# Kernel optimization log

Measured on AMD Instinct MI355X. Metric: run time of the kernel, lower is better.

The kernel has to match this reference:

```python
import jax, jax.numpy as jnp
import numpy as np

CLUSTER_TEMP = 5.0


def setup_inputs() -> dict:
    key = jax.random.key(0)
    ks = jax.random.split(key, 8)
    n, d_in, h, d, K = 50000, 512, 1024, 256, 64
    s = lambda f: 1.0 / np.sqrt(f)
    return {
        "x": jax.random.normal(ks[0], (n, d_in), dtype=jnp.float32),
        "W1": jax.random.normal(ks[1], (d_in, h), dtype=jnp.float32) * s(d_in),
        "b1": jnp.zeros((h,), jnp.float32),
        "W2": jax.random.normal(ks[2], (h, h), dtype=jnp.float32) * s(h),
        "b2": jnp.zeros((h,), jnp.float32),
        "W3": jax.random.normal(ks[3], (h, d), dtype=jnp.float32) * s(h),
        "b3": jnp.zeros((d,), jnp.float32),
        "mu_init": jax.random.normal(ks[4], (K, d), dtype=jnp.float32),
        "num_iter": 10,
    }


def reference(x, W1, b1, W2, b2, W3, b3, mu_init, num_iter):
    # MLP embed: ReLU on all but last layer
    h1 = jax.nn.relu(x @ W1 + b1)
    h2 = jax.nn.relu(h1 @ W2 + b2)
    embeds = h2 @ W3 + b3                      # [n, d]

    # row-wise L2 normalize (torch.diag(1/norm) @ data == row scaling)
    data = embeds / jnp.linalg.norm(embeds, axis=1, keepdims=True)

    def step(mu, _):
        dist = data @ mu.T                     # [n, K]
        r = jax.nn.softmax(CLUSTER_TEMP * dist, axis=1)
        cluster_r = r.sum(axis=0)              # [K]
        cluster_mean = jnp.einsum('nk,nd->kd', r, data)  # [K, d]
        new_mu = cluster_mean / cluster_r[:, None]       # diag(1/cluster_r) @ mean
        return new_mu, None

    mu, _ = jax.lax.scan(step, mu_init, None, length=num_iter)
    dist = data @ mu.T
    r = jax.nn.softmax(CLUSTER_TEMP * dist, axis=1)      # forward returns r only
    return r
```

## Files before the change

### kernel.cpp

```cpp
#include <hip/hip_runtime.h>
#include <math.h>

#define CLUSTER_TEMP 5.0f

typedef __attribute__((ext_vector_type(8))) short bf16x8;
typedef __attribute__((ext_vector_type(4))) float f32x4;

__device__ __forceinline__ unsigned short f2bf(float f) {
  unsigned u = __float_as_uint(f);
  u += 0x7fff + ((u >> 16) & 1);
  return (unsigned short)(u >> 16);
}
__device__ __forceinline__ float bf2f(unsigned short s) {
  return __uint_as_float((unsigned)s << 16);
}

typedef const __attribute__((address_space(1))) void* gas_t;
typedef __attribute__((address_space(3))) void* las_t;
__device__ __forceinline__ void gload16(const void* g, void* l) {
  __builtin_amdgcn_global_load_lds((gas_t)g, (las_t)l, 16, 0, 0);
}

__global__ __launch_bounds__(256)
void wprep(const float* __restrict__ W, unsigned short* __restrict__ hi,
           unsigned short* __restrict__ lo, int K, int N)
{
  __shared__ float tile[32][33];
  const int bx = blockIdx.x * 32;
  const int by = blockIdx.y * 32;
  const int tx = threadIdx.x, ty = threadIdx.y;
#pragma unroll
  for (int i = 0; i < 4; ++i)
    tile[ty + i*8][tx] = W[(size_t)(by + ty + i*8)*N + bx + tx];
  __syncthreads();
#pragma unroll
  for (int i = 0; i < 4; ++i) {
    const int nn = bx + ty + i*8;
    const int kk = by + tx;
    const float v = tile[tx][ty + i*8];
    const unsigned short h = f2bf(v);
    hi[(size_t)nn*K + kk] = h;
    lo[(size_t)nn*K + kk] = f2bf(v - bf2f(h));
  }
}

__global__ __launch_bounds__(256)
void xsplit(const float* __restrict__ x, unsigned short* __restrict__ xh,
            unsigned short* __restrict__ xl, long total4)
{
  long i = (long)blockIdx.x*256 + threadIdx.x;
  const long stride = (long)gridDim.x*256;
  for (; i < total4; i += stride) {
    float4 v = ((const float4*)x)[i];
    ushort4 h, lo;
    h.x = f2bf(v.x); lo.x = f2bf(v.x - bf2f(h.x));
    h.y = f2bf(v.y); lo.y = f2bf(v.y - bf2f(h.y));
    h.z = f2bf(v.z); lo.z = f2bf(v.z - bf2f(h.z));
    h.w = f2bf(v.w); lo.w = f2bf(v.w - bf2f(h.w));
    ((ushort4*)xh)[i] = h;
    ((ushort4*)xl)[i] = lo;
  }
}

template<bool RELU, bool PAIR_OUT>
__global__ __launch_bounds__(256, 2)
void gemm_pair(const unsigned short* __restrict__ Ah, const unsigned short* __restrict__ Al,
               const unsigned short* __restrict__ Bh, const unsigned short* __restrict__ Bl,
               const float* __restrict__ bias,
               unsigned short* __restrict__ Ch, unsigned short* __restrict__ Cl,
               float* __restrict__ Cf,
               int M, int N, int K)
{
  __shared__ unsigned short As_h[128][32];
  __shared__ unsigned short As_l[128][32];
  __shared__ unsigned short Bs_h[128][32];
  __shared__ unsigned short Bs_l[128][32];
  const int t = threadIdx.x, l = t & 63, w = t >> 6;
  const int wm = w >> 1, wn = w & 1;
  const int fr = l & 15, fq = l >> 4;

  const int gx = gridDim.x;
  const int total = gx * gridDim.y;
  const int flat = blockIdx.y * gx + blockIdx.x;
  const int q = total >> 3, rmd = total & 7;
  const int xcd = flat & 7, pos = flat >> 3;
  const int nid = (xcd < rmd ? xcd * (q + 1) : rmd * (q + 1) + (xcd - rmd) * q) + pos;
  const int row0 = (nid / gx) * 128;
  const int col0 = (nid % gx) * 128;

  const int srow = l >> 2;
  const int scol = (l & 3) * 8;

  f32x4 acc[4][4];
#pragma unroll
  for (int i = 0; i < 4; ++i)
#pragma unroll
    for (int j = 0; j < 4; ++j) {
      acc[i][j][0]=0.f; acc[i][j][1]=0.f; acc[i][j][2]=0.f; acc[i][j][3]=0.f;
    }

  for (int k0 = 0; k0 < K; k0 += 32) {
    __syncthreads();
#pragma unroll
    for (int j = 0; j < 2; ++j) {
      const int chunk = w*2 + j;
      const int rl = chunk*16 + srow;
      const int ra = min(row0 + rl, M-1);
      const size_t ao = (size_t)ra*K + k0 + scol;
      const size_t bo = (size_t)(col0 + rl)*K + k0 + scol;
      gload16(Ah + ao, &As_h[chunk*16][0]);
      gload16(Al + ao, &As_l[chunk*16][0]);
      gload16(Bh + bo, &Bs_h[chunk*16][0]);
      gload16(Bl + bo, &Bs_l[chunk*16][0]);
    }
    __syncthreads();

    bf16x8 ah[4], al[4], bh[4], bl[4];
#pragma unroll
    for (int i = 0; i < 4; ++i) {
      ah[i] = *(const bf16x8*)&As_h[wm*64 + i*16 + fr][fq*8];
      al[i] = *(const bf16x8*)&As_l[wm*64 + i*16 + fr][fq*8];
      bh[i] = *(const bf16x8*)&Bs_h[wn*64 + i*16 + fr][fq*8];
      bl[i] = *(const bf16x8*)&Bs_l[wn*64 + i*16 + fr][fq*8];
    }
#pragma unroll
    for (int i = 0; i < 4; ++i)
#pragma unroll
      for (int j = 0; j < 4; ++j) {
        acc[i][j] = __builtin_amdgcn_mfma_f32_16x16x32_bf16(ah[i], bh[j], acc[i][j], 0, 0, 0);
        acc[i][j] = __builtin_amdgcn_mfma_f32_16x16x32_bf16(ah[i], bl[j], acc[i][j], 0, 0, 0);
        acc[i][j] = __builtin_amdgcn_mfma_f32_16x16x32_bf16(al[i], bh[j], acc[i][j], 0, 0, 0);
      }
  }

  float bj[4];
#pragma unroll
  for (int j = 0; j < 4; ++j) bj[j] = bias[col0 + wn*64 + j*16 + fr];

#pragma unroll
  for (int i = 0; i < 4; ++i)
#pragma unroll
    for (int qq = 0; qq < 4; ++qq) {
      const int r = row0 + wm*64 + i*16 + fq*4 + qq;
      if (r < M) {
#pragma unroll
        for (int j = 0; j < 4; ++j) {
          float v = acc[i][j][qq] + bj[j];
          if constexpr (RELU) v = fmaxf(v, 0.f);
          const int cidx = col0 + wn*64 + j*16 + fr;
          if constexpr (PAIR_OUT) {
            const unsigned short h = f2bf(v);
            Ch[(size_t)r*N + cidx] = h;
            Cl[(size_t)r*N + cidx] = f2bf(v - bf2f(h));
          } else {
            Cf[(size_t)r*N + cidx] = v;
          }
        }
      }
    }
}

__global__ __launch_bounds__(256)
void normsplit(const float* __restrict__ E,
               unsigned short* __restrict__ dsph, unsigned short* __restrict__ dspl,
               unsigned short* __restrict__ dshT, unsigned short* __restrict__ dslT,
               int n, int nt)
{
  __shared__ float tile[64][260];
  __shared__ float nrm[4][64];
  __shared__ float invr[64];
  const int t = threadIdx.x;
  const int n0 = blockIdx.x * 64;
#pragma unroll
  for (int i = 0; i < 16; ++i) {
    const int flat = t + i*256;
    const int r = flat >> 6, c4 = (flat & 63) * 4;
    const int rg = min(n0 + r, n - 1);
    *(float4*)&tile[r][c4] = *(const float4*)(E + (size_t)rg*256 + c4);
  }
  __syncthreads();
  {
    const int r = t & 63, qq = t >> 6;
    float s = 0.f;
#pragma unroll
    for (int j = 0; j < 64; ++j) { const float v = tile[r][qq*64 + j]; s = fmaf(v, v, s); }
    nrm[qq][r] = s;
  }
  __syncthreads();
  if (t < 64) invr[t] = 1.0f / sqrtf(nrm[0][t] + nrm[1][t] + nrm[2][t] + nrm[3][t]);
  __syncthreads();
#pragma unroll
  for (int i = 0; i < 16; ++i) {
    const int flat = t + i*256;
    const int r = flat >> 6, c4 = (flat & 63) * 4;
    float4 v = *(const float4*)&tile[r][c4];
    const float iv = invr[r];
    v.x *= iv; v.y *= iv; v.z *= iv; v.w *= iv;
    ushort4 h, lo;
    h.x = f2bf(v.x); lo.x = f2bf(v.x - bf2f(h.x));
    h.y = f2bf(v.y); lo.y = f2bf(v.y - bf2f(h.y));
    h.z = f2bf(v.z); lo.z = f2bf(v.z - bf2f(h.z));
    h.w = f2bf(v.w); lo.w = f2bf(v.w - bf2f(h.w));
    const int rg = n0 + r;
    const int rb = rg >> 4, fr = rg & 15;
    const int ks = c4 >> 5, g = (c4 >> 3) & 3, j = c4 & 7;
    const size_t o = ((size_t)(rb*8 + ks)*64 + g*16 + fr)*8 + j;
    *(ushort4*)(dsph + o) = h;
    *(ushort4*)(dspl + o) = lo;
  }
  const int dd = t >> 3;
  const int nseg = t & 7;
#pragma unroll
  for (int dgrp = 0; dgrp < 8; ++dgrp) {
    const int d = dgrp*32 + dd;
    union { unsigned short s[8]; uint4 u; } hb, lb;
#pragma unroll
    for (int j = 0; j < 8; ++j) {
      const int r = nseg*8 + j;
      const float v = tile[r][d] * invr[r];
      const unsigned short h = f2bf(v);
      hb.s[j] = h; lb.s[j] = f2bf(v - bf2f(h));
    }
    *(uint4*)(dshT + (size_t)d*nt + n0 + nseg*8) = hb.u;
    *(uint4*)(dslT + (size_t)d*nt + n0 + nseg*8) = lb.u;
  }
}

__device__ __forceinline__ size_t mu_off(int k, int d) {
  return ((size_t)((k >> 4)*8 + (d >> 5))*64 + ((d >> 3) & 3)*16 + (k & 15))*8 + (d & 7);
}

__global__ __launch_bounds__(256)
void musplit0(const float* __restrict__ mu0, unsigned short* __restrict__ muPh,
              unsigned short* __restrict__ muPl)
{
  const int i = blockIdx.x*256 + threadIdx.x;
  const int k = i >> 8, d = i & 255;
  const float v = mu0[i];
  const unsigned short h = f2bf(v);
  const size_t o = mu_off(k, d);
  muPh[o] = h; muPl[o] = f2bf(v - bf2f(h));
}

template<bool FINAL>
__global__ __launch_bounds__(256, 2)
void cluster_iter(const unsigned short* __restrict__ dsph, const unsigned short* __restrict__ dspl,
                  const unsigned short* __restrict__ dshT, const unsigned short* __restrict__ dslT,
                  const unsigned short* __restrict__ muPh, const unsigned short* __restrict__ muPl,
                  float* __restrict__ acc_g, float* __restrict__ accr_g,
                  float* __restrict__ out, int n, int nt)
{
  __shared__ unsigned pt[64][132];
  __shared__ float crp[4][64];
  const int t = threadIdx.x, l = t & 63, w = t >> 6;
  const int fr = l & 15, g = l >> 4;
  const int base = blockIdx.x * 128;
  const int rb0 = (base >> 4) + 2*w;

  f32x4 dacc[2][4];
#pragma unroll
  for (int mf = 0; mf < 2; ++mf)
#pragma unroll
    for (int nf = 0; nf < 4; ++nf) {
      dacc[mf][nf][0]=0.f; dacc[mf][nf][1]=0.f; dacc[mf][nf][2]=0.f; dacc[mf][nf][3]=0.f;
    }
#pragma unroll
  for (int ks = 0; ks < 8; ++ks) {
    bf16x8 Ah[2], Al[2];
#pragma unroll
    for (int mf = 0; mf < 2; ++mf) {
      const size_t ao = ((size_t)((rb0 + mf)*8 + ks)*64 + l)*8;
      Ah[mf] = *(const bf16x8*)(dsph + ao);
      Al[mf] = *(const bf16x8*)(dspl + ao);
    }
#pragma unroll
    for (int nf = 0; nf < 4; ++nf) {
      const size_t bo = ((size_t)(nf*8 + ks)*64 + l)*8;
      const bf16x8 Bh = *(const bf16x8*)(muPh + bo);
      const bf16x8 Bl = *(const bf16x8*)(muPl + bo);
#pragma unroll
      for (int mf = 0; mf < 2; ++mf) {
        dacc[mf][nf] = __builtin_amdgcn_mfma_f32_16x16x32_bf16(Ah[mf], Bh, dacc[mf][nf], 0, 0, 0);
        dacc[mf][nf] = __builtin_amdgcn_mfma_f32_16x16x32_bf16(Ah[mf], Bl, dacc[mf][nf], 0, 0, 0);
        dacc[mf][nf] = __builtin_amdgcn_mfma_f32_16x16x32_bf16(Al[mf], Bh, dacc[mf][nf], 0, 0, 0);
      }
    }
  }

  float accr[4] = {0.f, 0.f, 0.f, 0.f};
#pragma unroll
  for (int mf = 0; mf < 2; ++mf) {
    float mx[4], se[4], p[4][4];
#pragma unroll
    for (int r = 0; r < 4; ++r) {
      mx[r] = fmaxf(fmaxf(dacc[mf][0][r], dacc[mf][1][r]),
                    fmaxf(dacc[mf][2][r], dacc[mf][3][r]));
#pragma unroll
      for (int off = 1; off < 16; off <<= 1) mx[r] = fmaxf(mx[r], __shfl_xor(mx[r], off));
      se[r] = 0.f;
    }
#pragma unroll
    for (int nf = 0; nf < 4; ++nf)
#pragma unroll
      for (int r = 0; r < 4; ++r) {
        p[nf][r] = __expf(CLUSTER_TEMP * (dacc[mf][nf][r] - mx[r]));
        se[r] += p[nf][r];
      }
#pragma unroll
    for (int r = 0; r < 4; ++r) {
#pragma unroll
      for (int off = 1; off < 16; off <<= 1) se[r] += __shfl_xor(se[r], off);
      se[r] = 1.0f / se[r];
    }
    if (FINAL) {
#pragma unroll
      for (int r = 0; r < 4; ++r) {
        const int rowg = base + 32*w + mf*16 + 4*g + r;
        if (rowg < n) {
#pragma unroll
          for (int nf = 0; nf < 4; ++nf)
            out[(size_t)rowg*64 + nf*16 + fr] = p[nf][r] * se[r];
        }
      }
    } else {
#pragma unroll
      for (int r = 0; r < 4; ++r) {
        const int rowg = base + 32*w + mf*16 + 4*g + r;
        const float sc = (rowg < n) ? se[r] : 0.f;
#pragma unroll
        for (int nf = 0; nf < 4; ++nf) {
          const float P = p[nf][r] * sc;
          accr[nf] += P;
          const unsigned short h = f2bf(P);
          const unsigned short lo = f2bf(P - bf2f(h));
          pt[nf*16 + fr][32*w + mf*16 + 4*g + r] = ((unsigned)h << 16) | (unsigned)lo;
        }
      }
    }
  }

  if (FINAL) return;

#pragma unroll
  for (int nf = 0; nf < 4; ++nf) {
    accr[nf] += __shfl_xor(accr[nf], 16);
    accr[nf] += __shfl_xor(accr[nf], 32);
  }
  if (l < 16) {
#pragma unroll
    for (int nf = 0; nf < 4; ++nf) crp[w][nf*16 + l] = accr[nf];
  }
  __syncthreads();

  f32x4 acc2[4][4];
#pragma unroll
  for (int i = 0; i < 4; ++i)
#pragma unroll
    for (int j = 0; j < 4; ++j) {
      acc2[i][j][0]=0.f; acc2[i][j][1]=0.f; acc2[i][j][2]=0.f; acc2[i][j][3]=0.f;
    }
#pragma unroll
  for (int ks = 0; ks < 4; ++ks) {
    bf16x8 Ph[4], Pl[4];
#pragma unroll
    for (int mf = 0; mf < 4; ++mf) {
      union { unsigned u[8]; uint4 v[2]; } uu;
      uu.v[0] = *(const uint4*)&pt[mf*16 + fr][ks*32 + 8*g];
      uu.v[1] = *(const uint4*)&pt[mf*16 + fr][ks*32 + 8*g + 4];
      union { unsigned short s[8]; bf16x8 v; } hh, ll;
#pragma unroll
      for (int j = 0; j < 8; ++j) {
        hh.s[j] = (unsigned short)(uu.u[j] >> 16);
        ll.s[j] = (unsigned short)(uu.u[j] & 0xffffu);
      }
      Ph[mf] = hh.v; Pl[mf] = ll.v;
    }
#pragma unroll
    for (int nf = 0; nf < 4; ++nf) {
      const size_t bo = (size_t)(64*w + nf*16 + fr)*nt + base + ks*32 + 8*g;
      const bf16x8 Bh = *(const bf16x8*)(dshT + bo);
      const bf16x8 Bl = *(const bf16x8*)(dslT + bo);
#pragma unroll
      for (int mf = 0; mf < 4; ++mf) {
        acc2[mf][nf] = __builtin_amdgcn_mfma_f32_16x16x32_bf16(Ph[mf], Bh, acc2[mf][nf], 0, 0, 0);
        acc2[mf][nf] = __builtin_amdgcn_mfma_f32_16x16x32_bf16(Ph[mf], Bl, acc2[mf][nf], 0, 0, 0);
        acc2[mf][nf] = __builtin_amdgcn_mfma_f32_16x16x32_bf16(Pl[mf], Bh, acc2[mf][nf], 0, 0, 0);
      }
    }
  }

#pragma unroll
  for (int mf = 0; mf < 4; ++mf)
#pragma unroll
    for (int nf = 0; nf < 4; ++nf)
#pragma unroll
      for (int r = 0; r < 4; ++r)
        atomicAdd(&acc_g[(size_t)(mf*16 + 4*g + r)*256 + 64*w + nf*16 + fr],
                  acc2[mf][nf][r]);
  if (t < 64)
    atomicAdd(&accr_g[t], crp[0][t] + crp[1][t] + crp[2][t] + crp[3][t]);
}

__global__ __launch_bounds__(256)
void musplit_it(float* __restrict__ acc_g, float* __restrict__ accr_g,
                unsigned short* __restrict__ muPh, unsigned short* __restrict__ muPl)
{
  const int k = blockIdx.x;
  const int d = threadIdx.x;
  const float r = accr_g[k];
  const float v = acc_g[(size_t)k*256 + d] / r;
  __syncthreads();
  const size_t o = mu_off(k, d);
  const unsigned short h = f2bf(v);
  muPh[o] = h; muPl[o] = f2bf(v - bf2f(h));
  acc_g[(size_t)k*256 + d] = 0.f;
  if (d == 0) accr_g[k] = 0.f;
}

extern "C" void kernel_launch(void* const* d_in, const int* in_sizes, int n_in,
                              void* d_out, int out_size, void* d_ws, size_t ws_size,
                              hipStream_t stream)
{
  const float* x   = (const float*)d_in[0];
  const float* W1  = (const float*)d_in[1];
  const float* b1  = (const float*)d_in[2];
  const float* W2  = (const float*)d_in[3];
  const float* b2  = (const float*)d_in[4];
  const float* W3  = (const float*)d_in[5];
  const float* b3  = (const float*)d_in[6];
  const float* mu0 = (const float*)d_in[7];
  const int DIN = 512, H = 1024, D = 256, ITERS = 10;
  const int n = in_sizes[0] / DIN;
  const int NP = ((n + 127) / 128) * 128;
  const int NT = (n + 64 + 255) & ~255;
  const int NBK = NP / 128;

  char* ws = (char*)d_ws;
  const size_t MB = 1024*1024;
  const size_t nH2 = (size_t)n * H * 2;
  unsigned short* h1h = (unsigned short*)ws;
  unsigned short* h1l = (unsigned short*)(ws + nH2);
  unsigned short* xh  = (unsigned short*)(ws + 2*nH2);
  unsigned short* xl  = (unsigned short*)(ws + 2*nH2 + (size_t)n*DIN*2);
  unsigned short* h2h = (unsigned short*)(ws + 2*nH2);
  unsigned short* h2l = (unsigned short*)(ws + 3*nH2);
  float* data = (float*)ws;
  unsigned short* dsph = (unsigned short*)(ws + 52*MB);
  unsigned short* dspl = (unsigned short*)(ws + 78*MB);
  unsigned short* dshT = (unsigned short*)(ws + 104*MB);
  unsigned short* dslT = (unsigned short*)(ws + 130*MB);
  float* acc_g  = (float*)(ws + 182*MB);
  float* accr_g = acc_g + 16384;
  unsigned short* muPh = (unsigned short*)(ws + 183*MB);
  unsigned short* muPl = (unsigned short*)(ws + 184*MB);

  unsigned short* w1th = (unsigned short*)d_out;
  unsigned short* w1tl = w1th + (size_t)H*DIN;
  unsigned short* w2th = w1tl + (size_t)H*DIN;
  unsigned short* w2tl = w2th + (size_t)H*H;
  unsigned short* w3th = w2tl + (size_t)H*H;
  unsigned short* w3tl = w3th + (size_t)D*H;

  hipMemsetAsync(acc_g, 0, (16384 + 64) * sizeof(float), stream);

  wprep<<<dim3(H/32, DIN/32), dim3(32,8), 0, stream>>>(W1, w1th, w1tl, DIN, H);
  wprep<<<dim3(H/32, H/32),   dim3(32,8), 0, stream>>>(W2, w2th, w2tl, H, H);
  wprep<<<dim3(D/32, H/32),   dim3(32,8), 0, stream>>>(W3, w3th, w3tl, H, D);
  xsplit<<<dim3(2048), dim3(256), 0, stream>>>(x, xh, xl, (long)n*DIN/4);

  const int gy = (n + 127) / 128;
  gemm_pair<true,  true ><<<dim3(H/128, gy), 256, 0, stream>>>(
      xh, xl, w1th, w1tl, b1, h1h, h1l, nullptr, n, H, DIN);
  gemm_pair<true,  true ><<<dim3(H/128, gy), 256, 0, stream>>>(
      h1h, h1l, w2th, w2tl, b2, h2h, h2l, nullptr, n, H, H);
  gemm_pair<false, false><<<dim3(D/128, gy), 256, 0, stream>>>(
      h2h, h2l, w3th, w3tl, b3, nullptr, nullptr, data, n, D, H);

  normsplit<<<dim3(NT/64), dim3(256), 0, stream>>>(data, dsph, dspl, dshT, dslT, n, NT);
  musplit0<<<dim3(64), dim3(256), 0, stream>>>(mu0, muPh, muPl);

  for (int it = 0; it < ITERS; ++it) {
    cluster_iter<false><<<dim3(NBK), dim3(256), 0, stream>>>(
        dsph, dspl, dshT, dslT, muPh, muPl, acc_g, accr_g, nullptr, n, NT);
    musplit_it<<<dim3(64), dim3(256), 0, stream>>>(acc_g, accr_g, muPh, muPl);
  }
  cluster_iter<true><<<dim3(NBK), dim3(256), 0, stream>>>(
      dsph, dspl, dshT, dslT, muPh, muPl, nullptr, nullptr, (float*)d_out, n, NT);
}
```

Baseline: 1.223 ms.

## Fuse input fp32 split into first GEMM and spread cluster atomics over copies

The first MLP GEMM now reads fp32 x directly and splits it into bf16 hi/lo inside the tile load, which removes the separate xsplit pass and its write and reread of two bf16 copies of x. The cluster iteration now spreads its atomic accumulation across 8 partial buffers chosen by block index, and musplit_it sums and clears all of them. This is meant to cut atomic contention on one 64x256 accumulator. In exchange the A-tile load in GEMM1 becomes a synchronous register path instead of direct global-to-LDS loads, and musplit does more reads and writes.

```diff
diff --git a/kernel.cpp b/kernel.cpp
--- a/kernel.cpp
+++ b/kernel.cpp
@@ -2,6 +2,7 @@
 #include <math.h>
 
 #define CLUSTER_TEMP 5.0f
+#define NSPL 8
 
 typedef __attribute__((ext_vector_type(8))) short bf16x8;
 typedef __attribute__((ext_vector_type(4))) float f32x4;
@@ -44,27 +45,10 @@
   }
 }
 
-__global__ __launch_bounds__(256)
-void xsplit(const float* __restrict__ x, unsigned short* __restrict__ xh,
-            unsigned short* __restrict__ xl, long total4)
-{
-  long i = (long)blockIdx.x*256 + threadIdx.x;
-  const long stride = (long)gridDim.x*256;
-  for (; i < total4; i += stride) {
-    float4 v = ((const float4*)x)[i];
-    ushort4 h, lo;
-    h.x = f2bf(v.x); lo.x = f2bf(v.x - bf2f(h.x));
-    h.y = f2bf(v.y); lo.y = f2bf(v.y - bf2f(h.y));
-    h.z = f2bf(v.z); lo.z = f2bf(v.z - bf2f(h.z));
-    h.w = f2bf(v.w); lo.w = f2bf(v.w - bf2f(h.w));
-    ((ushort4*)xh)[i] = h;
-    ((ushort4*)xl)[i] = lo;
-  }
-}
-
-template<bool RELU, bool PAIR_OUT>
+template<int INMODE, bool RELU, bool PAIR_OUT>
 __global__ __launch_bounds__(256, 2)
-void gemm_pair(const unsigned short* __restrict__ Ah, const unsigned short* __restrict__ Al,
+void gemm_pair(const float* __restrict__ Af,
+               const unsigned short* __restrict__ Ah, const unsigned short* __restrict__ Al,
                const unsigned short* __restrict__ Bh, const unsigned short* __restrict__ Bl,
                const float* __restrict__ bias,
                unsigned short* __restrict__ Ch, unsigned short* __restrict__ Cl,
@@ -101,17 +85,42 @@
 
   for (int k0 = 0; k0 < K; k0 += 32) {
     __syncthreads();
-#pragma unroll
-    for (int j = 0; j < 2; ++j) {
-      const int chunk = w*2 + j;
-      const int rl = chunk*16 + srow;
-      const int ra = min(row0 + rl, M-1);
-      const size_t ao = (size_t)ra*K + k0 + scol;
-      const size_t bo = (size_t)(col0 + rl)*K + k0 + scol;
-      gload16(Ah + ao, &As_h[chunk*16][0]);
-      gload16(Al + ao, &As_l[chunk*16][0]);
-      gload16(Bh + bo, &Bs_h[chunk*16][0]);
-      gload16(Bl + bo, &Bs_l[chunk*16][0]);
+    if constexpr (INMODE == 0) {
+#pragma unroll
+      for (int i = 0; i < 4; ++i) {
+        const int f = t + i*256;
+        const int r = f >> 3, c4 = (f & 7) * 4;
+        const int ra = min(row0 + r, M - 1);
+        const float4 v = *(const float4*)(Af + (size_t)ra*K + k0 + c4);
+        ushort4 hv, lv;
+        hv.x = f2bf(v.x); lv.x = f2bf(v.x - bf2f(hv.x));
+        hv.y = f2bf(v.y); lv.y = f2bf(v.y - bf2f(hv.y));
+        hv.z = f2bf(v.z); lv.z = f2bf(v.z - bf2f(hv.z));
+        hv.w = f2bf(v.w); lv.w = f2bf(v.w - bf2f(hv.w));
+        *(ushort4*)&As_h[r][c4] = hv;
+        *(ushort4*)&As_l[r][c4] = lv;
+      }
+#pragma unroll
+      for (int j = 0; j < 2; ++j) {
+        const int chunk = w*2 + j;
+        const int rl = chunk*16 + srow;
+        const size_t bo = (size_t)(col0 + rl)*K + k0 + scol;
+        gload16(Bh + bo, &Bs_h[chunk*16][0]);
+        gload16(Bl + bo, &Bs_l[chunk*16][0]);
+      }
+    } else {
+#pragma unroll
+      for (int j = 0; j < 2; ++j) {
+        const int chunk = w*2 + j;
+        const int rl = chunk*16 + srow;
+        const int ra = min(row0 + rl, M-1);
+        const size_t ao = (size_t)ra*K + k0 + scol;
+        const size_t bo = (size_t)(col0 + rl)*K + k0 + scol;
+        gload16(Ah + ao, &As_h[chunk*16][0]);
+        gload16(Al + ao, &As_l[chunk*16][0]);
+        gload16(Bh + bo, &Bs_h[chunk*16][0]);
+        gload16(Bl + bo, &Bs_l[chunk*16][0]);
+      }
     }
     __syncthreads();
 
@@ -389,32 +398,40 @@
     }
   }
 
+  float* accs = acc_g + (size_t)(blockIdx.x & (NSPL-1)) * 16448;
 #pragma unroll
   for (int mf = 0; mf < 4; ++mf)
 #pragma unroll
     for (int nf = 0; nf < 4; ++nf)
 #pragma unroll
       for (int r = 0; r < 4; ++r)
-        atomicAdd(&acc_g[(size_t)(mf*16 + 4*g + r)*256 + 64*w + nf*16 + fr],
+        atomicAdd(&accs[(size_t)(mf*16 + 4*g + r)*256 + 64*w + nf*16 + fr],
                   acc2[mf][nf][r]);
   if (t < 64)
-    atomicAdd(&accr_g[t], crp[0][t] + crp[1][t] + crp[2][t] + crp[3][t]);
+    atomicAdd(&accs[16384 + t], crp[0][t] + crp[1][t] + crp[2][t] + crp[3][t]);
 }
 
 __global__ __launch_bounds__(256)
-void musplit_it(float* __restrict__ acc_g, float* __restrict__ accr_g,
+void musplit_it(float* __restrict__ acc_g,
                 unsigned short* __restrict__ muPh, unsigned short* __restrict__ muPl)
 {
   const int k = blockIdx.x;
   const int d = threadIdx.x;
-  const float r = accr_g[k];
-  const float v = acc_g[(size_t)k*256 + d] / r;
+  float v = 0.f, r = 0.f;
+#pragma unroll
+  for (int c = 0; c < NSPL; ++c) {
+    v += acc_g[(size_t)c*16448 + (size_t)k*256 + d];
+    r += acc_g[(size_t)c*16448 + 16384 + k];
+  }
+  v /= r;
   __syncthreads();
   const size_t o = mu_off(k, d);
   const unsigned short h = f2bf(v);
   muPh[o] = h; muPl[o] = f2bf(v - bf2f(h));
-  acc_g[(size_t)k*256 + d] = 0.f;
-  if (d == 0) accr_g[k] = 0.f;
+#pragma unroll
+  for (int c = 0; c < NSPL; ++c)
+    acc_g[(size_t)c*16448 + (size_t)k*256 + d] = 0.f;
+  if (d < NSPL) acc_g[(size_t)d*16448 + 16384 + k] = 0.f;
 }
 
 extern "C" void kernel_launch(void* const* d_in, const int* in_sizes, int n_in,
@@ -440,8 +457,6 @@
   const size_t nH2 = (size_t)n * H * 2;
   unsigned short* h1h = (unsigned short*)ws;
   unsigned short* h1l = (unsigned short*)(ws + nH2);
-  unsigned short* xh  = (unsigned short*)(ws + 2*nH2);
-  unsigned short* xl  = (unsigned short*)(ws + 2*nH2 + (size_t)n*DIN*2);
   unsigned short* h2h = (unsigned short*)(ws + 2*nH2);
   unsigned short* h2l = (unsigned short*)(ws + 3*nH2);
   float* data = (float*)ws;
@@ -450,7 +465,6 @@
   unsigned short* dshT = (unsigned short*)(ws + 104*MB);
   unsigned short* dslT = (unsigned short*)(ws + 130*MB);
   float* acc_g  = (float*)(ws + 182*MB);
-  float* accr_g = acc_g + 16384;
   unsigned short* muPh = (unsigned short*)(ws + 183*MB);
   unsigned short* muPl = (unsigned short*)(ws + 184*MB);
 
@@ -461,28 +475,27 @@
   unsigned short* w3th = w2tl + (size_t)H*H;
   unsigned short* w3tl = w3th + (size_t)D*H;
 
-  hipMemsetAsync(acc_g, 0, (16384 + 64) * sizeof(float), stream);
+  hipMemsetAsync(acc_g, 0, (size_t)NSPL * 16448 * sizeof(float), stream);
 
   wprep<<<dim3(H/32, DIN/32), dim3(32,8), 0, stream>>>(W1, w1th, w1tl, DIN, H);
   wprep<<<dim3(H/32, H/32),   dim3(32,8), 0, stream>>>(W2, w2th, w2tl, H, H);
   wprep<<<dim3(D/32, H/32),   dim3(32,8), 0, stream>>>(W3, w3th, w3tl, H, D);
-  xsplit<<<dim3(2048), dim3(256), 0, stream>>>(x, xh, xl, (long)n*DIN/4);
 
   const int gy = (n + 127) / 128;
-  gemm_pair<true,  true ><<<dim3(H/128, gy), 256, 0, stream>>>(
-      xh, xl, w1th, w1tl, b1, h1h, h1l, nullptr, n, H, DIN);
-  gemm_pair<true,  true ><<<dim3(H/128, gy), 256, 0, stream>>>(
-      h1h, h1l, w2th, w2tl, b2, h2h, h2l, nullptr, n, H, H);
-  gemm_pair<false, false><<<dim3(D/128, gy), 256, 0, stream>>>(
-      h2h, h2l, w3th, w3tl, b3, nullptr, nullptr, data, n, D, H);
+  gemm_pair<0, true,  true ><<<dim3(H/128, gy), 256, 0, stream>>>(
+      x, nullptr, nullptr, w1th, w1tl, b1, h1h, h1l, nullptr, n, H, DIN);
+  gemm_pair<1, true,  true ><<<dim3(H/128, gy), 256, 0, stream>>>(
+      nullptr, h1h, h1l, w2th, w2tl, b2, h2h, h2l, nullptr, n, H, H);
+  gemm_pair<1, false, false><<<dim3(D/128, gy), 256, 0, stream>>>(
+      nullptr, h2h, h2l, w3th, w3tl, b3, nullptr, nullptr, data, n, D, H);
 
   normsplit<<<dim3(NT/64), dim3(256), 0, stream>>>(data, dsph, dspl, dshT, dslT, n, NT);
   musplit0<<<dim3(64), dim3(256), 0, stream>>>(mu0, muPh, muPl);
 
   for (int it = 0; it < ITERS; ++it) {
     cluster_iter<false><<<dim3(NBK), dim3(256), 0, stream>>>(
-        dsph, dspl, dshT, dslT, muPh, muPl, acc_g, accr_g, nullptr, n, NT);
-    musplit_it<<<dim3(64), dim3(256), 0, stream>>>(acc_g, accr_g, muPh, muPl);
+        dsph, dspl, dshT, dslT, muPh, muPl, acc_g, nullptr, nullptr, n, NT);
+    musplit_it<<<dim3(64), dim3(256), 0, stream>>>(acc_g, muPh, muPl);
   }
   cluster_iter<true><<<dim3(NBK), dim3(256), 0, stream>>>(
       dsph, dspl, dshT, dslT, muPh, muPl, nullptr, nullptr, (float*)d_out, n, NT);
```

New measurement: 1.141 ms. -6.8%, faster.
